# Optimization experiments

Hardware: AMD Instinct MI355X
Metric: run time of the kernel (lower is better)

## Reference

```python
import jax, jax.numpy as jnp
import numpy as np

EMBED_DIM = 1024
NUM_HEADS = 16
HEAD_DIM = EMBED_DIM // NUM_HEADS
SCALE = HEAD_DIM ** -0.5


def setup_inputs() -> dict:
    key = jax.random.key(0)
    ks = jax.random.split(key, 12)
    B, T, S, C = 4, 2048, 2048, EMBED_DIM
    inp = {
        "query": jax.random.normal(ks[0], (B, T, C), dtype=jnp.float32),
        "key": jax.random.normal(ks[1], (B, S, C), dtype=jnp.float32),
        "value": jax.random.normal(ks[2], (B, S, C), dtype=jnp.float32),
        "attn_mask": jnp.zeros((T, S), dtype=jnp.float32),
        "key_padding_mask": jnp.zeros((B, S), dtype=bool),
    }
    std = C ** -0.5
    for i, name in enumerate(["q", "k", "v", "out"]):
        inp[f"W{name}"] = jax.random.normal(ks[3 + i], (C, C), dtype=jnp.float32) * std
        inp[f"b{name}"] = jnp.zeros((C,), dtype=jnp.float32)
    return inp


def reference(query, key, value, attn_mask, key_padding_mask,
              Wq, bq, Wk, bk, Wv, bv, Wout, bout):
    B, T, C = query.shape
    S = key.shape[1]
    H, D = NUM_HEADS, HEAD_DIM
    # linear projections (torch Linear: x @ W.T + b)
    q = (query @ Wq.T + bq).reshape(B, T, H, D).transpose(0, 2, 1, 3)  # (B,H,T,D)
    k = (key @ Wk.T + bk).reshape(B, S, H, D).transpose(0, 2, 1, 3)    # (B,H,S,D)
    v = (value @ Wv.T + bv).reshape(B, S, H, D).transpose(0, 2, 1, 3)  # (B,H,S,D)
    # scaled dot-product attention with full (B,H,T,S) scores (faithful to source)
    scores = jnp.einsum("bhtd,bhsd->bhts", q, k) * SCALE
    scores = scores + attn_mask[None, None, :, :]
    scores = jnp.where(key_padding_mask[:, None, None, :], -jnp.inf, scores)
    weights = jax.nn.softmax(scores, axis=-1)
    attn_out = jnp.einsum("bhts,bhsd->bhtd", weights, v)
    attn_out = attn_out.transpose(0, 2, 1, 3).reshape(B, T, C)
    return attn_out @ Wout.T + bout
```

## Files before the change

### kernel.cpp

```cpp
#include <hip/hip_runtime.h>
#include <stdint.h>

#define NB 4
#define NT 2048
#define NC 1024
#define NH 16
#define ND 64
#define ACT_ELEMS (8388608ull)
#define W_ELEMS   (1048576ull)

typedef __attribute__((ext_vector_type(8))) short short8;
typedef __attribute__((ext_vector_type(4))) float f32x4;
typedef __attribute__((ext_vector_type(2))) unsigned int u32x2;

__device__ __forceinline__ unsigned short f2bf(float x) {
    unsigned int u = __float_as_uint(x);
    u += 0x7fffu + ((u >> 16) & 1u);
    return (unsigned short)(u >> 16);
}
__device__ __forceinline__ unsigned int f2bf2(float a, float b) {
    return (unsigned int)f2bf(a) | ((unsigned int)f2bf(b) << 16);
}

#if defined(__has_builtin)
#if __has_builtin(__builtin_amdgcn_global_load_lds)
#define HAS_GLDS 1
#endif
#endif

__device__ __forceinline__ void gl_lds16(const unsigned short* g, unsigned short* lds_wave_base) {
#ifdef HAS_GLDS
    __builtin_amdgcn_global_load_lds(
        (const __attribute__((address_space(1))) void*)g,
        (__attribute__((address_space(3))) void*)lds_wave_base, 16, 0, 0);
#else
    int lane = threadIdx.x & 63;
    *(short8*)(lds_wave_base + lane * 8) = *(const short8*)g;
#endif
}

__global__ __launch_bounds__(256) void cvt_all(const float* __restrict__ q,
                                               const float* __restrict__ k,
                                               const float* __restrict__ v,
                                               const float* __restrict__ wq,
                                               const float* __restrict__ wk,
                                               const float* __restrict__ wv,
                                               const float* __restrict__ wo,
                                               unsigned short* __restrict__ xb,
                                               unsigned short* __restrict__ wb) {
    int bid = blockIdx.x;
    const float* src;
    unsigned short* dst;
    int chunk;
    if (bid < 12288) {
        int z = bid >> 12; chunk = bid & 4095;
        src = (z == 0) ? q : (z == 1) ? k : v;
        dst = xb + (size_t)z * ACT_ELEMS;
    } else {
        int z = (bid - 12288) >> 9; chunk = (bid - 12288) & 511;
        src = (z == 0) ? wq : (z == 1) ? wk : (z == 2) ? wv : wo;
        dst = wb + (size_t)z * W_ELEMS;
    }
    size_t i = (size_t)chunk * 2048 + (size_t)threadIdx.x * 8;
    f32x4 f0 = *(const f32x4*)(src + i);
    f32x4 f1 = *(const f32x4*)(src + i + 4);
    u32x2 p0 = {f2bf2(f0[0], f0[1]), f2bf2(f0[2], f0[3])};
    u32x2 p1 = {f2bf2(f1[0], f1[1]), f2bf2(f1[2], f1[3])};
    *(u32x2*)(dst + i) = p0;
    *(u32x2*)(dst + i + 4) = p1;
}

template <int STORE>
__device__ __forceinline__ void gemm_body(const unsigned short* __restrict__ A,
                                          const unsigned short* __restrict__ W,
                                          const float* __restrict__ bias,
                                          unsigned short* __restrict__ dstb,
                                          float* __restrict__ dstf) {
    __shared__ unsigned short As[128 * 32];
    __shared__ unsigned short Bs[128 * 32];

    const int tid  = threadIdx.x;
    const int m0   = blockIdx.x * 128;
    const int n0   = blockIdx.y * 128;
    const int lane = tid & 63;
    const int wave = tid >> 6;
    const int col  = lane & 15;
    const int quad = lane >> 4;
    const int wr   = wave >> 1;
    const int wc   = wave & 1;

    f32x4 acc[4][4];
    const f32x4 fzero = {0.f, 0.f, 0.f, 0.f};
#pragma unroll
    for (int i = 0; i < 4; ++i)
#pragma unroll
        for (int j = 0; j < 4; ++j) acc[i][j] = fzero;

    for (int k0 = 0; k0 < NC; k0 += 32) {
#pragma unroll
        for (int r = 0; r < 2; ++r) {
            int g   = r * 256 + tid;
            int row = g >> 2;
            int cc  = (g & 3) * 8;
            unsigned short* abase = As + (size_t)(r * 2048 + wave * 512);
            unsigned short* bbase = Bs + (size_t)(r * 2048 + wave * 512);
            gl_lds16(A + (size_t)(m0 + row) * NC + k0 + cc, abase);
            gl_lds16(W + (size_t)(n0 + row) * NC + k0 + cc, bbase);
        }
        __syncthreads();

        short8 af[4], bf[4];
#pragma unroll
        for (int i = 0; i < 4; ++i)
            af[i] = *(const short8*)&As[(wr * 64 + i * 16 + col) * 32 + quad * 8];
#pragma unroll
        for (int j = 0; j < 4; ++j)
            bf[j] = *(const short8*)&Bs[(wc * 64 + j * 16 + col) * 32 + quad * 8];
#pragma unroll
        for (int i = 0; i < 4; ++i)
#pragma unroll
            for (int j = 0; j < 4; ++j)
                acc[i][j] = __builtin_amdgcn_mfma_f32_16x16x32_bf16(af[i], bf[j], acc[i][j], 0, 0, 0);
        __syncthreads();
    }

#pragma unroll
    for (int j = 0; j < 4; ++j) {
        int n = n0 + wc * 64 + j * 16 + col;
        float bv = bias[n];
#pragma unroll
        for (int i = 0; i < 4; ++i) {
#pragma unroll
            for (int r = 0; r < 4; ++r) {
                int m = m0 + wr * 64 + i * 16 + quad * 4 + r;
                float val = acc[i][j][r] + bv;
                if (STORE == 0) {
                    size_t idx = ((size_t)((m >> 11) * NH + (n >> 6)) * NT + (m & 2047)) * ND + (n & 63);
                    dstb[idx] = f2bf(val);
                } else {
                    dstf[(size_t)m * NC + n] = val;
                }
            }
        }
    }
}

__global__ __launch_bounds__(256) void proj_kernel(const unsigned short* __restrict__ xb,
                                                   const unsigned short* __restrict__ wb,
                                                   const float* __restrict__ b0,
                                                   const float* __restrict__ b1,
                                                   const float* __restrict__ b2,
                                                   unsigned short* __restrict__ qkv) {
    int z = blockIdx.z;
    const float* bias = (z == 0) ? b0 : (z == 1) ? b1 : b2;
    gemm_body<0>(xb + (size_t)z * ACT_ELEMS, wb + (size_t)z * W_ELEMS, bias,
                 qkv + (size_t)z * ACT_ELEMS, nullptr);
}

__global__ __launch_bounds__(256) void outproj_kernel(const unsigned short* __restrict__ ao,
                                                      const unsigned short* __restrict__ w,
                                                      const float* __restrict__ bias,
                                                      float* __restrict__ out) {
    gemm_body<1>(ao, w, bias, nullptr, out);
}

__global__ __launch_bounds__(256, 2) void attn_kernel(const unsigned short* __restrict__ q,
                                                      const unsigned short* __restrict__ k,
                                                      const unsigned short* __restrict__ v,
                                                      const float* __restrict__ amask,
                                                      const unsigned char* __restrict__ kpm,
                                                      unsigned short* __restrict__ ao) {
    __shared__ unsigned short Ks[64 * 72];
    __shared__ unsigned short Vt[64 * 72];
    __shared__ unsigned short Pl[4][64 * 72];

    const int tid  = threadIdx.x;
    const int lane = tid & 63;
    const int wave = tid >> 6;
    const int col  = lane & 15;
    const int quad = lane >> 4;

    const int b  = blockIdx.z;
    const int h  = blockIdx.y;
    const int t0 = blockIdx.x * 256;

    const size_t headbase = (size_t)(b * NH + h) * NT * ND;

    short8 qf[4][2];
#pragma unroll
    for (int tg = 0; tg < 4; ++tg) {
        const unsigned short* qr =
            q + headbase + (size_t)(t0 + wave * 64 + tg * 16 + col) * ND + quad * 8;
        qf[tg][0] = *(const short8*)qr;
        qf[tg][1] = *(const short8*)(qr + 32);
    }

    const f32x4 fzero = {0.f, 0.f, 0.f, 0.f};
    f32x4 O[4][4];
#pragma unroll
    for (int tg = 0; tg < 4; ++tg)
#pragma unroll
        for (int dg = 0; dg < 4; ++dg) O[tg][dg] = fzero;
    float lsum[4] = {0.f, 0.f, 0.f, 0.f};

    const int ksr = tid >> 2;
    const int ksc = (tid & 3) * 8;
    const int vsp = tid & 31;
    const int vd0 = (tid >> 5) * 8;
    unsigned short* Plw = Pl[wave];

    for (int s0 = 0; s0 < NT; s0 += 64) {
        {
            const unsigned short* kp_ = k + headbase + (size_t)(s0 + ksr) * ND;
            *(short8*)&Ks[ksr * 72 + ksc]      = *(const short8*)(kp_ + ksc);
            *(short8*)&Ks[ksr * 72 + ksc + 32] = *(const short8*)(kp_ + ksc + 32);
        }
        {
            int s_ = vsp * 2;
            const unsigned short* vp = v + headbase + (size_t)(s0 + s_) * ND + vd0;
            short8 va = *(const short8*)vp;
            short8 vb = *(const short8*)(vp + ND);
            unsigned int* dst = (unsigned int*)Vt;
#pragma unroll
            for (int i = 0; i < 8; ++i) {
                unsigned int pk = (unsigned int)(unsigned short)va[i] |
                                  ((unsigned int)(unsigned short)vb[i] << 16);
                dst[(vd0 + i) * 36 + vsp] = pk;
            }
        }
        __syncthreads();

#pragma unroll
        for (int sg = 0; sg < 4; ++sg) {
            const unsigned short* kb_ = &Ks[(sg * 16 + col) * 72 + quad * 8];
            short8 af0 = *(const short8*)kb_;
            short8 af1 = *(const short8*)(kb_ + 32);
            unsigned int kb = *(const unsigned int*)(kpm + b * NT + s0 + sg * 16 + quad * 4);
#pragma unroll
            for (int tg = 0; tg < 4; ++tg) {
                f32x4 z = fzero;
                z = __builtin_amdgcn_mfma_f32_16x16x32_bf16(af0, qf[tg][0], z, 0, 0, 0);
                z = __builtin_amdgcn_mfma_f32_16x16x32_bf16(af1, qf[tg][1], z, 0, 0, 0);
                int t = t0 + wave * 64 + tg * 16 + col;
                f32x4 mv = *(const f32x4*)(amask + (size_t)t * NT + s0 + sg * 16 + quad * 4);
                float p[4];
#pragma unroll
                for (int r = 0; r < 4; ++r) {
                    float scv = z[r] * 0.125f + mv[r];
                    if ((kb >> (r * 8)) & 0xffu) scv = -INFINITY;
                    p[r] = __expf(scv);
                }
                lsum[tg] += (p[0] + p[1]) + (p[2] + p[3]);
                u32x2 pkv;
                pkv[0] = f2bf2(p[0], p[1]);
                pkv[1] = f2bf2(p[2], p[3]);
                *(u32x2*)&Plw[(tg * 16 + col) * 72 + sg * 16 + quad * 4] = pkv;
            }
        }

        short8 pf[4][2];
#pragma unroll
        for (int tg = 0; tg < 4; ++tg)
#pragma unroll
            for (int sk = 0; sk < 2; ++sk)
                pf[tg][sk] = *(const short8*)&Plw[(tg * 16 + col) * 72 + sk * 32 + quad * 8];
#pragma unroll
        for (int dg = 0; dg < 4; ++dg) {
            short8 vf0 = *(const short8*)&Vt[(dg * 16 + col) * 72 + quad * 8];
            short8 vf1 = *(const short8*)&Vt[(dg * 16 + col) * 72 + 32 + quad * 8];
#pragma unroll
            for (int tg = 0; tg < 4; ++tg) {
                O[tg][dg] = __builtin_amdgcn_mfma_f32_16x16x32_bf16(pf[tg][0], vf0, O[tg][dg], 0, 0, 0);
                O[tg][dg] = __builtin_amdgcn_mfma_f32_16x16x32_bf16(pf[tg][1], vf1, O[tg][dg], 0, 0, 0);
            }
        }
        __syncthreads();
    }

    float linv[4];
#pragma unroll
    for (int tg = 0; tg < 4; ++tg) {
        float s = lsum[tg];
        s += __shfl_xor(s, 16);
        s += __shfl_xor(s, 32);
        linv[tg] = 1.0f / s;
    }
#pragma unroll
    for (int tg = 0; tg < 4; ++tg) {
#pragma unroll
        for (int r = 0; r < 4; ++r) {
            float inv = __shfl(linv[tg], quad * 4 + r);
            int t = t0 + wave * 64 + tg * 16 + quad * 4 + r;
#pragma unroll
            for (int dg = 0; dg < 4; ++dg) {
                size_t idx = (size_t)(b * NT + t) * NC + h * ND + dg * 16 + col;
                ao[idx] = f2bf(O[tg][dg][r] * inv);
            }
        }
    }
}

extern "C" void kernel_launch(void* const* d_in, const int* in_sizes, int n_in,
                              void* d_out, int out_size, void* d_ws, size_t ws_size,
                              hipStream_t stream) {
    const float* query = (const float*)d_in[0];
    const float* key_  = (const float*)d_in[1];
    const float* value = (const float*)d_in[2];
    const float* amask = (const float*)d_in[3];
    const unsigned char* kpm = (const unsigned char*)d_in[4];
    const float* Wq = (const float*)d_in[5];
    const float* bq = (const float*)d_in[6];
    const float* Wk = (const float*)d_in[7];
    const float* bk = (const float*)d_in[8];
    const float* Wv = (const float*)d_in[9];
    const float* bv = (const float*)d_in[10];
    const float* Wo = (const float*)d_in[11];
    const float* bo = (const float*)d_in[12];
    float* out = (float*)d_out;

    unsigned short* ws = (unsigned short*)d_ws;
    unsigned short* xb  = ws;
    unsigned short* qb  = ws + 3 * ACT_ELEMS;
    unsigned short* wb  = ws + 6 * ACT_ELEMS;
    unsigned short* aob = xb;

    cvt_all<<<14336, 256, 0, stream>>>(query, key_, value, Wq, Wk, Wv, Wo, xb, wb);

    dim3 pg(64, 8, 3);
    proj_kernel<<<pg, 256, 0, stream>>>(xb, wb, bq, bk, bv, qb);

    dim3 ag(NT / 256, NH, NB);
    attn_kernel<<<ag, 256, 0, stream>>>(qb, qb + ACT_ELEMS, qb + 2 * ACT_ELEMS,
                                        amask, kpm, aob);

    dim3 og(64, 8, 1);
    outproj_kernel<<<og, 256, 0, stream>>>(aob, wb + 3 * W_ELEMS, bo, out);
}
```

Measured before the change: 453.6 us.

## Restructure attention: register-resident P, double-buffered V, direct K loads, smaller tiles

The attention kernel now keeps the softmax probabilities in registers and feeds them straight into the PV MFMA by computing transposed (V^T·P) products, so the per-wave P buffer in LDS goes away. K fragments are read directly from global memory instead of being staged in LDS. V^T is double-buffered so the next tile's load overlaps the current compute. The key padding mask is precomputed once as an additive float array in LDS, the bf16 pack uses a cheaper perm-based rounding, and the output is written with vector stores. Each block now covers 128 query rows instead of 256, with occupancy raised to 3 blocks; this lowers K/V reuse per block and adds uncached-style global K reads, and the changed rounding (round-half-up instead of round-to-even) slightly alters numerics.

```diff
diff --git a/kernel.cpp b/kernel.cpp
--- a/kernel.cpp
+++ b/kernel.cpp
@@ -20,6 +20,11 @@
 }
 __device__ __forceinline__ unsigned int f2bf2(float a, float b) {
     return (unsigned int)f2bf(a) | ((unsigned int)f2bf(b) << 16);
+}
+__device__ __forceinline__ unsigned int bfpack(float a, float b) {
+    unsigned int ua = __float_as_uint(a) + 0x8000u;
+    unsigned int ub = __float_as_uint(b) + 0x8000u;
+    return __builtin_amdgcn_perm(ub, ua, 0x07060302u);
 }
 
 #if defined(__has_builtin)
@@ -164,15 +169,14 @@
     gemm_body<1>(ao, w, bias, nullptr, out);
 }
 
-__global__ __launch_bounds__(256, 2) void attn_kernel(const unsigned short* __restrict__ q,
+__global__ __launch_bounds__(256, 3) void attn_kernel(const unsigned short* __restrict__ q,
                                                       const unsigned short* __restrict__ k,
                                                       const unsigned short* __restrict__ v,
                                                       const float* __restrict__ amask,
                                                       const unsigned char* __restrict__ kpm,
                                                       unsigned short* __restrict__ ao) {
-    __shared__ unsigned short Ks[64 * 72];
-    __shared__ unsigned short Vt[64 * 72];
-    __shared__ unsigned short Pl[4][64 * 72];
+    __shared__ unsigned short Vt[2][64 * 72];
+    __shared__ float kpmF[NT];
 
     const int tid  = threadIdx.x;
     const int lane = tid & 63;
@@ -182,120 +186,133 @@
 
     const int b  = blockIdx.z;
     const int h  = blockIdx.y;
-    const int t0 = blockIdx.x * 256;
+    const int t0 = blockIdx.x * 128;
 
     const size_t headbase = (size_t)(b * NH + h) * NT * ND;
 
-    short8 qf[4][2];
-#pragma unroll
-    for (int tg = 0; tg < 4; ++tg) {
+    {
+        const unsigned char* kp8 = kpm + b * NT + tid * 8;
+        f32x4 r0, r1;
+#pragma unroll
+        for (int j = 0; j < 4; ++j) r0[j] = kp8[j] ? -INFINITY : 0.0f;
+#pragma unroll
+        for (int j = 0; j < 4; ++j) r1[j] = kp8[4 + j] ? -INFINITY : 0.0f;
+        *(f32x4*)&kpmF[tid * 8]     = r0;
+        *(f32x4*)&kpmF[tid * 8 + 4] = r1;
+    }
+
+    short8 qf[2][2];
+#pragma unroll
+    for (int tg = 0; tg < 2; ++tg) {
         const unsigned short* qr =
-            q + headbase + (size_t)(t0 + wave * 64 + tg * 16 + col) * ND + quad * 8;
+            q + headbase + (size_t)(t0 + wave * 32 + tg * 16 + col) * ND + quad * 8;
         qf[tg][0] = *(const short8*)qr;
         qf[tg][1] = *(const short8*)(qr + 32);
     }
 
     const f32x4 fzero = {0.f, 0.f, 0.f, 0.f};
-    f32x4 O[4][4];
-#pragma unroll
-    for (int tg = 0; tg < 4; ++tg)
+    f32x4 O[2][4];
+#pragma unroll
+    for (int tg = 0; tg < 2; ++tg)
 #pragma unroll
         for (int dg = 0; dg < 4; ++dg) O[tg][dg] = fzero;
-    float lsum[4] = {0.f, 0.f, 0.f, 0.f};
-
-    const int ksr = tid >> 2;
-    const int ksc = (tid & 3) * 8;
+    float lsum[2] = {0.f, 0.f};
+
     const int vsp = tid & 31;
     const int vd0 = (tid >> 5) * 8;
-    unsigned short* Plw = Pl[wave];
-
+
+    {
+        const unsigned short* vp = v + headbase + (size_t)(vsp * 2) * ND + vd0;
+        short8 va = *(const short8*)vp;
+        short8 vb2 = *(const short8*)(vp + ND);
+        unsigned int* dst = (unsigned int*)Vt[0];
+#pragma unroll
+        for (int i = 0; i < 8; ++i)
+            dst[(vd0 + i) * 36 + vsp] =
+                (unsigned int)(unsigned short)va[i] | ((unsigned int)(unsigned short)vb2[i] << 16);
+    }
+    __syncthreads();
+
+    int buf = 0;
     for (int s0 = 0; s0 < NT; s0 += 64) {
-        {
-            const unsigned short* kp_ = k + headbase + (size_t)(s0 + ksr) * ND;
-            *(short8*)&Ks[ksr * 72 + ksc]      = *(const short8*)(kp_ + ksc);
-            *(short8*)&Ks[ksr * 72 + ksc + 32] = *(const short8*)(kp_ + ksc + 32);
-        }
-        {
-            int s_ = vsp * 2;
-            const unsigned short* vp = v + headbase + (size_t)(s0 + s_) * ND + vd0;
-            short8 va = *(const short8*)vp;
-            short8 vb = *(const short8*)(vp + ND);
-            unsigned int* dst = (unsigned int*)Vt;
-#pragma unroll
-            for (int i = 0; i < 8; ++i) {
-                unsigned int pk = (unsigned int)(unsigned short)va[i] |
-                                  ((unsigned int)(unsigned short)vb[i] << 16);
-                dst[(vd0 + i) * 36 + vsp] = pk;
+        short8 vna, vnb;
+        const bool last = (s0 + 64 >= NT);
+        if (!last) {
+            const unsigned short* vp = v + headbase + (size_t)(s0 + 64 + vsp * 2) * ND + vd0;
+            vna = *(const short8*)vp;
+            vnb = *(const short8*)(vp + ND);
+        }
+
+        const unsigned short* vbuf = Vt[buf];
+#pragma unroll
+        for (int sh = 0; sh < 2; ++sh) {
+            unsigned int pku[2][4];
+#pragma unroll
+            for (int sp = 0; sp < 2; ++sp) {
+                int sg = sh * 2 + sp;
+                const unsigned short* kr =
+                    k + headbase + (size_t)(s0 + sg * 16 + col) * ND + quad * 8;
+                short8 kf0 = *(const short8*)kr;
+                short8 kf1 = *(const short8*)(kr + 32);
+                f32x4 kb4 = *(const f32x4*)&kpmF[s0 + sg * 16 + quad * 4];
+#pragma unroll
+                for (int tg = 0; tg < 2; ++tg) {
+                    f32x4 z = fzero;
+                    z = __builtin_amdgcn_mfma_f32_16x16x32_bf16(kf0, qf[tg][0], z, 0, 0, 0);
+                    z = __builtin_amdgcn_mfma_f32_16x16x32_bf16(kf1, qf[tg][1], z, 0, 0, 0);
+                    int t = t0 + wave * 32 + tg * 16 + col;
+                    f32x4 mv = *(const f32x4*)(amask + (size_t)t * NT + s0 + sg * 16 + quad * 4);
+                    float p0 = __expf(z[0] * 0.125f + mv[0] + kb4[0]);
+                    float p1 = __expf(z[1] * 0.125f + mv[1] + kb4[1]);
+                    float p2 = __expf(z[2] * 0.125f + mv[2] + kb4[2]);
+                    float p3 = __expf(z[3] * 0.125f + mv[3] + kb4[3]);
+                    lsum[tg] += (p0 + p1) + (p2 + p3);
+                    pku[tg][sp * 2]     = bfpack(p0, p1);
+                    pku[tg][sp * 2 + 1] = bfpack(p2, p3);
+                }
             }
+            union { unsigned int u[4]; short8 s8; } pb0, pb1;
+#pragma unroll
+            for (int i = 0; i < 4; ++i) { pb0.u[i] = pku[0][i]; pb1.u[i] = pku[1][i]; }
+#pragma unroll
+            for (int dg = 0; dg < 4; ++dg) {
+                const unsigned short* vr = vbuf + (dg * 16 + col) * 72 + sh * 32 + quad * 4;
+                union { uint64_t u[2]; short8 s8; } af;
+                af.u[0] = *(const uint64_t*)vr;
+                af.u[1] = *(const uint64_t*)(vr + 16);
+                O[0][dg] = __builtin_amdgcn_mfma_f32_16x16x32_bf16(af.s8, pb0.s8, O[0][dg], 0, 0, 0);
+                O[1][dg] = __builtin_amdgcn_mfma_f32_16x16x32_bf16(af.s8, pb1.s8, O[1][dg], 0, 0, 0);
+            }
+        }
+
+        if (!last) {
+            unsigned int* dst = (unsigned int*)Vt[buf ^ 1];
+#pragma unroll
+            for (int i = 0; i < 8; ++i)
+                dst[(vd0 + i) * 36 + vsp] =
+                    (unsigned int)(unsigned short)vna[i] | ((unsigned int)(unsigned short)vnb[i] << 16);
         }
         __syncthreads();
-
-#pragma unroll
-        for (int sg = 0; sg < 4; ++sg) {
-            const unsigned short* kb_ = &Ks[(sg * 16 + col) * 72 + quad * 8];
-            short8 af0 = *(const short8*)kb_;
-            short8 af1 = *(const short8*)(kb_ + 32);
-            unsigned int kb = *(const unsigned int*)(kpm + b * NT + s0 + sg * 16 + quad * 4);
-#pragma unroll
-            for (int tg = 0; tg < 4; ++tg) {
-                f32x4 z = fzero;
-                z = __builtin_amdgcn_mfma_f32_16x16x32_bf16(af0, qf[tg][0], z, 0, 0, 0);
-                z = __builtin_amdgcn_mfma_f32_16x16x32_bf16(af1, qf[tg][1], z, 0, 0, 0);
-                int t = t0 + wave * 64 + tg * 16 + col;
-                f32x4 mv = *(const f32x4*)(amask + (size_t)t * NT + s0 + sg * 16 + quad * 4);
-                float p[4];
-#pragma unroll
-                for (int r = 0; r < 4; ++r) {
-                    float scv = z[r] * 0.125f + mv[r];
-                    if ((kb >> (r * 8)) & 0xffu) scv = -INFINITY;
-                    p[r] = __expf(scv);
-                }
-                lsum[tg] += (p[0] + p[1]) + (p[2] + p[3]);
-                u32x2 pkv;
-                pkv[0] = f2bf2(p[0], p[1]);
-                pkv[1] = f2bf2(p[2], p[3]);
-                *(u32x2*)&Plw[(tg * 16 + col) * 72 + sg * 16 + quad * 4] = pkv;
-            }
-        }
-
-        short8 pf[4][2];
-#pragma unroll
-        for (int tg = 0; tg < 4; ++tg)
-#pragma unroll
-            for (int sk = 0; sk < 2; ++sk)
-                pf[tg][sk] = *(const short8*)&Plw[(tg * 16 + col) * 72 + sk * 32 + quad * 8];
-#pragma unroll
-        for (int dg = 0; dg < 4; ++dg) {
-            short8 vf0 = *(const short8*)&Vt[(dg * 16 + col) * 72 + quad * 8];
-            short8 vf1 = *(const short8*)&Vt[(dg * 16 + col) * 72 + 32 + quad * 8];
-#pragma unroll
-            for (int tg = 0; tg < 4; ++tg) {
-                O[tg][dg] = __builtin_amdgcn_mfma_f32_16x16x32_bf16(pf[tg][0], vf0, O[tg][dg], 0, 0, 0);
-                O[tg][dg] = __builtin_amdgcn_mfma_f32_16x16x32_bf16(pf[tg][1], vf1, O[tg][dg], 0, 0, 0);
-            }
-        }
-        __syncthreads();
-    }
-
-    float linv[4];
-#pragma unroll
-    for (int tg = 0; tg < 4; ++tg) {
+        buf ^= 1;
+    }
+
+    float linv[2];
+#pragma unroll
+    for (int tg = 0; tg < 2; ++tg) {
         float s = lsum[tg];
         s += __shfl_xor(s, 16);
         s += __shfl_xor(s, 32);
         linv[tg] = 1.0f / s;
     }
 #pragma unroll
-    for (int tg = 0; tg < 4; ++tg) {
-#pragma unroll
-        for (int r = 0; r < 4; ++r) {
-            float inv = __shfl(linv[tg], quad * 4 + r);
-            int t = t0 + wave * 64 + tg * 16 + quad * 4 + r;
-#pragma unroll
-            for (int dg = 0; dg < 4; ++dg) {
-                size_t idx = (size_t)(b * NT + t) * NC + h * ND + dg * 16 + col;
-                ao[idx] = f2bf(O[tg][dg][r] * inv);
-            }
+    for (int tg = 0; tg < 2; ++tg) {
+        int t = t0 + wave * 32 + tg * 16 + col;
+#pragma unroll
+        for (int dg = 0; dg < 4; ++dg) {
+            u32x2 w;
+            w[0] = bfpack(O[tg][dg][0] * linv[tg], O[tg][dg][1] * linv[tg]);
+            w[1] = bfpack(O[tg][dg][2] * linv[tg], O[tg][dg][3] * linv[tg]);
+            *(u32x2*)(ao + (size_t)(b * NT + t) * NC + h * ND + dg * 16 + quad * 4) = w;
         }
     }
 }
@@ -329,7 +346,7 @@
     dim3 pg(64, 8, 3);
     proj_kernel<<<pg, 256, 0, stream>>>(xb, wb, bq, bk, bv, qb);
 
-    dim3 ag(NT / 256, NH, NB);
+    dim3 ag(NT / 128, NH, NB);
     attn_kernel<<<ag, 256, 0, stream>>>(qb, qb + ACT_ELEMS, qb + 2 * ACT_ELEMS,
                                         amask, kpm, aob);
 
```

After: 542.7 us. +19.6%, slower.
